# Kernel tuning notes

Measured on AMD Instinct MI355X. Metric: run time of the kernel, lower is better.

## Reference

```python
import jax, jax.numpy as jnp
import numpy as np


def setup_inputs() -> dict:
    key = jax.random.key(0)
    ks = jax.random.split(key, 12)
    S, B, I, H = 1024, 64, 1024, 1024
    stdv = 1.0 / np.sqrt(H)
    def u(k, shape):
        return jax.random.uniform(k, shape, jnp.float32, -stdv, stdv)
    return {
        "input": jax.random.normal(ks[0], (S, B, I), jnp.float32),
        "w_ih_r": u(ks[1], (H, I)),
        "w_hh_r": jax.random.normal(ks[2], (H, H), jnp.float32) * stdv,
        "w_ih_z": u(ks[3], (H, I)),
        "w_hh_z": jax.random.normal(ks[4], (H, H), jnp.float32) * stdv,
        "w_ih_n": u(ks[5], (H, I)),
        "w_hh_n": jax.random.normal(ks[6], (H, H), jnp.float32) * stdv,
        "b_ih_r": u(ks[7], (H,)),
        "b_hh_r": jnp.zeros((H,), jnp.float32),
        "b_ih_z": u(ks[8], (H,)),
        "b_hh_z": jnp.zeros((H,), jnp.float32),
        "b_ih_n": u(ks[9], (H,)),
        "b_hh_n": jnp.zeros((H,), jnp.float32),
    }


def _gru_forward(input, w_ih_r, w_hh_r, w_ih_z, w_hh_z, w_ih_n, w_hh_n,
                 b_ih_r, b_hh_r, b_ih_z, b_hh_z, b_ih_n, b_hh_n):
    S, B, _ = input.shape
    H = w_hh_r.shape[0]
    # Precompute input projections for all timesteps (large batched GEMMs).
    xr = jnp.einsum('sbi,hi->sbh', input, w_ih_r) + b_ih_r  # [S,B,H]
    xz = jnp.einsum('sbi,hi->sbh', input, w_ih_z) + b_ih_z
    xn = jnp.einsum('sbi,hi->sbh', input, w_ih_n) + b_ih_n

    h0 = jnp.zeros((B, H), input.dtype)

    def step(h, xs):
        xr_t, xz_t, xn_t = xs
        r = jax.nn.sigmoid(xr_t + h @ w_hh_r.T + b_hh_r)
        z = jax.nn.sigmoid(xz_t + h @ w_hh_z.T + b_hh_z)
        n = jnp.tanh(xn_t + (r * h) @ w_hh_n.T + b_hh_n)
        h_new = (1.0 - z) * n + z * h
        return h_new, h_new

    h_n, output = jax.lax.scan(step, h0, (xr, xz, xn))
    return output, h_n  # [S,B,H], [B,H]


def reference(input, w_ih_r, w_hh_r, w_ih_z, w_hh_z, w_ih_n, w_hh_n,
              b_ih_r, b_hh_r, b_ih_z, b_hh_z, b_ih_n, b_hh_n):
    return _gru_forward(input, w_ih_r, w_hh_r, w_ih_z, w_hh_z, w_ih_n, w_hh_n,
                        b_ih_r, b_hh_r, b_ih_z, b_hh_z, b_ih_n, b_hh_n)
```

## Files before the change

kernel.cpp:

```cpp
#include <hip/hip_runtime.h>
#include <hip/hip_bf16.h>

typedef __bf16 bf16_t;
typedef __bf16 bf16x8 __attribute__((ext_vector_type(8)));
typedef float  f32x4  __attribute__((ext_vector_type(4)));
typedef unsigned long long u64;

#define S_LEN 1024
#define NBLK  64
#define FLAG_STRIDE 64

__device__ inline f32x4 mfma16(bf16x8 a, bf16x8 b, f32x4 c) {
  return __builtin_amdgcn_mfma_f32_16x16x32_bf16(a, b, c, 0, 0, 0);
}
__device__ inline float fsigmoid(float x) {
  x = fmaxf(-30.f, fminf(30.f, x));
  return 1.f / (1.f + __expf(-x));
}
__device__ inline float ftanh(float x) {
  x = fmaxf(-15.f, fminf(15.f, x));
  float e = __expf(2.f * x);
  return (e - 1.f) / (e + 1.f);
}

__device__ inline void st_coh_bf16(bf16_t* p, float v) {
  bf16_t b = (bf16_t)v;
  __hip_atomic_store((unsigned short*)p, __builtin_bit_cast(unsigned short, b),
                     __ATOMIC_RELAXED, __HIP_MEMORY_SCOPE_AGENT);
}

__device__ __forceinline__ bf16x8 ld_coh(const bf16_t* p) {
  f32x4 r;
  asm volatile("global_load_dwordx4 %0, %1, off sc0 sc1" : "=v"(r) : "v"(p));
  return __builtin_bit_cast(bf16x8, r);
}

__global__ void k_cast_x(const float* __restrict__ x, bf16_t* __restrict__ xb, int n8) {
  int i = blockIdx.x * blockDim.x + threadIdx.x;
  if (i >= n8) return;
  const float4* p = (const float4*)(x + (size_t)i * 8);
  float4 a = p[0], b = p[1];
  bf16x8 o;
  o[0]=(bf16_t)a.x; o[1]=(bf16_t)a.y; o[2]=(bf16_t)a.z; o[3]=(bf16_t)a.w;
  o[4]=(bf16_t)b.x; o[5]=(bf16_t)b.y; o[6]=(bf16_t)b.z; o[7]=(bf16_t)b.w;
  *(bf16x8*)(xb + (size_t)i * 8) = o;
}

__global__ void k_prep_w(const float* __restrict__ wihr, const float* __restrict__ whhr,
                         const float* __restrict__ wihz, const float* __restrict__ whhz,
                         const float* __restrict__ wihn, const float* __restrict__ whhn,
                         const float* __restrict__ bihr, const float* __restrict__ bhhr,
                         const float* __restrict__ bihz, const float* __restrict__ bhhz,
                         const float* __restrict__ bihn, const float* __restrict__ bhhn,
                         bf16_t* __restrict__ wih, bf16_t* __restrict__ whh,
                         float* __restrict__ bias) {
  int i = blockIdx.x * blockDim.x + threadIdx.x;
  const int M = 1024 * 1024;
  if (i < M) {
    wih[i]       = (bf16_t)wihr[i];
    wih[M + i]   = (bf16_t)wihz[i];
    wih[2*M + i] = (bf16_t)wihn[i];
    whh[i]       = (bf16_t)whhr[i];
    whh[M + i]   = (bf16_t)whhz[i];
    whh[2*M + i] = (bf16_t)whhn[i];
  }
  if (i < 1024) {
    bias[i]        = bihr[i] + bhhr[i];
    bias[1024 + i] = bihz[i] + bhhz[i];
    bias[2048 + i] = bihn[i] + bhhn[i];
  }
}

__global__ __launch_bounds__(256) void k_gemm(
    const bf16_t* __restrict__ A, const bf16_t* __restrict__ B,
    const float* __restrict__ bias,
    bf16_t* __restrict__ xrz, float* __restrict__ xn)
{
  __shared__ __align__(16) bf16_t As[128 * 32];
  __shared__ __align__(16) bf16_t Bs[128 * 32];
  const int tid  = threadIdx.x;
  const int lane = tid & 63;
  const int wid  = tid >> 6;
  const int wm   = wid & 1, wn = wid >> 1;
  const int quad = lane >> 4, l15 = lane & 15;
  const int m0 = blockIdx.x * 128;
  const int f0 = blockIdx.y * 128;

  const int r0 = tid >> 2,         o0 = (tid & 3) * 8;
  const int r1 = (tid + 256) >> 2, o1 = ((tid + 256) & 3) * 8;

  const bf16_t* Ag = A + (size_t)m0 * 1024;
  const bf16_t* Bg = B + (size_t)f0 * 1024;

  f32x4 acc[4][4] = {};

  bf16x8 pa0 = *(const bf16x8*)(Ag + r0 * 1024 + o0);
  bf16x8 pa1 = *(const bf16x8*)(Ag + r1 * 1024 + o1);
  bf16x8 pb0 = *(const bf16x8*)(Bg + r0 * 1024 + o0);
  bf16x8 pb1 = *(const bf16x8*)(Bg + r1 * 1024 + o1);

  for (int k0 = 0; k0 < 1024; k0 += 32) {
    __syncthreads();
    *(bf16x8*)&As[r0 * 32 + o0] = pa0;
    *(bf16x8*)&As[r1 * 32 + o1] = pa1;
    *(bf16x8*)&Bs[r0 * 32 + o0] = pb0;
    *(bf16x8*)&Bs[r1 * 32 + o1] = pb1;
    __syncthreads();
    if (k0 + 32 < 1024) {
      const bf16_t* Ag2 = Ag + k0 + 32;
      const bf16_t* Bg2 = Bg + k0 + 32;
      pa0 = *(const bf16x8*)(Ag2 + r0 * 1024 + o0);
      pa1 = *(const bf16x8*)(Ag2 + r1 * 1024 + o1);
      pb0 = *(const bf16x8*)(Bg2 + r0 * 1024 + o0);
      pb1 = *(const bf16x8*)(Bg2 + r1 * 1024 + o1);
    }
    bf16x8 af[4], bfr[4];
#pragma unroll
    for (int t = 0; t < 4; t++) {
      af[t]  = *(const bf16x8*)&As[(wm * 64 + t * 16 + l15) * 32 + quad * 8];
      bfr[t] = *(const bf16x8*)&Bs[(wn * 64 + t * 16 + l15) * 32 + quad * 8];
    }
#pragma unroll
    for (int mt = 0; mt < 4; mt++)
#pragma unroll
      for (int nt = 0; nt < 4; nt++)
        acc[mt][nt] = mfma16(af[mt], bfr[nt], acc[mt][nt]);
  }

  float bcol[4];
#pragma unroll
  for (int nt = 0; nt < 4; nt++) bcol[nt] = bias[f0 + wn * 64 + nt * 16 + l15];

  const bool is_n = (blockIdx.y >= 16);
#pragma unroll
  for (int mt = 0; mt < 4; mt++) {
#pragma unroll
    for (int nt = 0; nt < 4; nt++) {
#pragma unroll
      for (int j = 0; j < 4; j++) {
        int m = m0 + wm * 64 + mt * 16 + quad * 4 + j;
        int f = f0 + wn * 64 + nt * 16 + l15;
        float v = acc[mt][nt][j] + bcol[nt];
        if (!is_n) xrz[(size_t)m * 2048 + f] = (bf16_t)v;
        else       xn[(size_t)m * 1024 + (f - 2048)] = v;
      }
    }
  }
}

__global__ void k_zero_flags(unsigned* f) {
  for (int i = threadIdx.x; i < NBLK * FLAG_STRIDE; i += 256) f[i] = 0;
}

__device__ inline void gridbar(unsigned* flags, int bid, unsigned p) {
  asm volatile("s_waitcnt vmcnt(0)" ::: "memory");
  __syncthreads();
  if (threadIdx.x == 0)
    __hip_atomic_store(&flags[bid * FLAG_STRIDE], p, __ATOMIC_RELAXED,
                       __HIP_MEMORY_SCOPE_AGENT);
  if (threadIdx.x < NBLK) {
    while (__hip_atomic_load(&flags[threadIdx.x * FLAG_STRIDE], __ATOMIC_RELAXED,
                             __HIP_MEMORY_SCOPE_AGENT) < p)
      __builtin_amdgcn_s_sleep(1);
  }
  __syncthreads();
}

__global__ __launch_bounds__(256, 1) void k_gru(
    const bf16_t* __restrict__ xrz,
    const bf16_t* __restrict__ whh,
    float* __restrict__ out,
    bf16_t* __restrict__ hb,
    bf16_t* __restrict__ rh, unsigned* __restrict__ flags)
{
  __shared__ __align__(16) bf16_t wl[48 * 1032];
  const int tid  = threadIdx.x;
  const int bid  = blockIdx.x;
  const int lane = tid & 63;
  const int wid  = tid >> 6;
  const int quad = lane >> 4, l15 = lane & 15;

  for (int i = tid; i < 48 * 128; i += 256) {
    int row = i >> 7;
    int c   = (i & 127) * 8;
    int gr  = (row >> 4) * 1024 + bid * 16 + (row & 15);
    *(bf16x8*)&wl[row * 1032 + c] = *(const bf16x8*)&whh[(size_t)gr * 1024 + c];
  }
  for (int i = tid; i < 64 * 4; i += 256) {
    int b = i >> 2, c = i & 3;
    __hip_atomic_store((u64*)(hb + (size_t)b * 1024 + bid * 16) + c, 0ull,
                       __ATOMIC_RELAXED, __HIP_MEMORY_SCOPE_AGENT);
  }
  gridbar(flags, bid, 1);

  const int abase = (wid * 16 + l15) * 1024 + quad * 8;
  const int fg = bid * 16 + l15;
  unsigned p = 2;

  float hreg[4] = {0.f, 0.f, 0.f, 0.f};
  float xr_pf[4], xz_pf[4], xn_pf[4];
#pragma unroll
  for (int j = 0; j < 4; j++) {
    int b = wid * 16 + quad * 4 + j;
    xr_pf[j] = (float)xrz[(size_t)b * 2048 + fg];
    xz_pf[j] = (float)xrz[(size_t)b * 2048 + 1024 + fg];
    xn_pf[j] = out[(size_t)b * 1024 + fg];
  }

  for (int t = 0; t < S_LEN; t++) {
    const int mrow = t * 64;

    bf16x8 hbuf[32];
    {
      const bf16_t* hrow = hb + abase;
#pragma unroll
      for (int kk = 0; kk < 32; kk++) hbuf[kk] = ld_coh(hrow + kk * 32);
    }
    f32x4 ar = {}, az = {};
    asm volatile("s_waitcnt vmcnt(16)" ::: "memory");
    __builtin_amdgcn_sched_barrier(0);
#pragma unroll
    for (int kk = 0; kk < 16; kk++) {
      bf16x8 br = *(const bf16x8*)&wl[l15 * 1032 + kk * 32 + quad * 8];
      bf16x8 bz = *(const bf16x8*)&wl[(16 + l15) * 1032 + kk * 32 + quad * 8];
      ar = mfma16(hbuf[kk], br, ar);
      az = mfma16(hbuf[kk], bz, az);
    }
    asm volatile("s_waitcnt vmcnt(0)" ::: "memory");
    __builtin_amdgcn_sched_barrier(0);
#pragma unroll
    for (int kk = 16; kk < 32; kk++) {
      bf16x8 br = *(const bf16x8*)&wl[l15 * 1032 + kk * 32 + quad * 8];
      bf16x8 bz = *(const bf16x8*)&wl[(16 + l15) * 1032 + kk * 32 + quad * 8];
      ar = mfma16(hbuf[kk], br, ar);
      az = mfma16(hbuf[kk], bz, az);
    }
    float zreg[4];
#pragma unroll
    for (int j = 0; j < 4; j++) {
      int b = wid * 16 + quad * 4 + j;
      float rv = fsigmoid(xr_pf[j] + ar[j]);
      float zv = fsigmoid(xz_pf[j] + az[j]);
      zreg[j] = zv;
      st_coh_bf16(&rh[b * 1024 + fg], rv * hreg[j]);
    }
    gridbar(flags, bid, p); p++;

    bf16x8 rbuf[32];
    {
      const bf16_t* rrow = rh + abase;
#pragma unroll
      for (int kk = 0; kk < 32; kk++) rbuf[kk] = ld_coh(rrow + kk * 32);
    }
    f32x4 an = {};
    asm volatile("s_waitcnt vmcnt(16)" ::: "memory");
    __builtin_amdgcn_sched_barrier(0);
#pragma unroll
    for (int kk = 0; kk < 16; kk++) {
      bf16x8 bn = *(const bf16x8*)&wl[(32 + l15) * 1032 + kk * 32 + quad * 8];
      an = mfma16(rbuf[kk], bn, an);
    }
    asm volatile("s_waitcnt vmcnt(0)" ::: "memory");
    __builtin_amdgcn_sched_barrier(0);
    float xn_cur[4];
#pragma unroll
    for (int j = 0; j < 4; j++) xn_cur[j] = xn_pf[j];
    if (t + 1 < S_LEN) {
#pragma unroll
      for (int j = 0; j < 4; j++) {
        int b = wid * 16 + quad * 4 + j;
        xr_pf[j] = (float)xrz[(size_t)(mrow + 64 + b) * 2048 + fg];
        xz_pf[j] = (float)xrz[(size_t)(mrow + 64 + b) * 2048 + 1024 + fg];
        xn_pf[j] = out[(size_t)(mrow + 64 + b) * 1024 + fg];
      }
    }
#pragma unroll
    for (int kk = 16; kk < 32; kk++) {
      bf16x8 bn = *(const bf16x8*)&wl[(32 + l15) * 1032 + kk * 32 + quad * 8];
      an = mfma16(rbuf[kk], bn, an);
    }
#pragma unroll
    for (int j = 0; j < 4; j++) {
      int b = wid * 16 + quad * 4 + j;
      size_t oix = (size_t)(mrow + b) * 1024 + fg;
      float nv  = ftanh(xn_cur[j] + an[j]);
      float hv  = (1.f - zreg[j]) * nv + zreg[j] * hreg[j];
      hreg[j] = hv;
      out[oix] = hv;
      st_coh_bf16(&hb[b * 1024 + fg], hv);
      if (t == S_LEN - 1) out[(size_t)S_LEN * 64 * 1024 + b * 1024 + fg] = hv;
    }
    if (t + 1 < S_LEN) { gridbar(flags, bid, p); p++; }
  }
}

extern "C" void kernel_launch(void* const* d_in, const int* in_sizes, int n_in,
                              void* d_out, int out_size, void* d_ws, size_t ws_size,
                              hipStream_t stream) {
  const float* x    = (const float*)d_in[0];
  const float* wihr = (const float*)d_in[1];
  const float* whhr = (const float*)d_in[2];
  const float* wihz = (const float*)d_in[3];
  const float* whhz = (const float*)d_in[4];
  const float* wihn = (const float*)d_in[5];
  const float* whhn = (const float*)d_in[6];
  const float* bihr = (const float*)d_in[7];
  const float* bhhr = (const float*)d_in[8];
  const float* bihz = (const float*)d_in[9];
  const float* bhhz = (const float*)d_in[10];
  const float* bihn = (const float*)d_in[11];
  const float* bhhn = (const float*)d_in[12];
  float* out = (float*)d_out;

  char* w = (char*)d_ws;
  bf16_t*  Xb    = (bf16_t*)(w);
  bf16_t*  xrz   = (bf16_t*)(w + 134217728);
  bf16_t*  wih   = (bf16_t*)(w + 402653184);
  bf16_t*  whh   = (bf16_t*)(w + 408944640);
  float*   bias  = (float*) (w + 415236096);
  unsigned* flags = (unsigned*)(w + 415248384);
  bf16_t*  hb    = (bf16_t*)(w + 415510528);
  bf16_t*  rh    = (bf16_t*)(w + 415641600);

  k_cast_x<<<dim3(8388608 / 256), dim3(256), 0, stream>>>(x, Xb, 8388608);
  k_prep_w<<<dim3(1048576 / 256), dim3(256), 0, stream>>>(
      wihr, whhr, wihz, whhz, wihn, whhn,
      bihr, bhhr, bihz, bhhz, bihn, bhhn, wih, whh, bias);
  k_gemm<<<dim3(512, 24), dim3(256), 0, stream>>>(Xb, wih, bias, xrz, out);
  k_zero_flags<<<dim3(1), dim3(256), 0, stream>>>(flags);
  k_gru<<<dim3(NBLK), dim3(256), 0, stream>>>(xrz, whh, out, hb, rh, flags);
}
```

Measured before the change: 13.60 ms.

## Replace block-wide grid barrier with per-wave flag barriers and split arrive/wait

Replaces the block-level grid barrier (syncthreads plus one flag per block) with per-wavefront flags. Each wave publishes its own flag and polls only the matching flags of the other blocks' same-index wave, using a wave-wide all-reduce and no __syncthreads. This works because each wave only consumes the batch rows its counterpart waves produce. The second barrier per step is split into arrive and wait, so the next timestep's xr/xz/xn prefetch loads are issued between them. The intent is to remove intra-block sync overhead and hide prefetch latency behind barrier waiting, at the cost of four times as many flags and more subtle correctness reasoning.

```diff
diff --git a/kernel.cpp b/kernel.cpp
--- a/kernel.cpp
+++ b/kernel.cpp
@@ -8,7 +8,7 @@
 
 #define S_LEN 1024
 #define NBLK  64
-#define FLAG_STRIDE 64
+#define FLAG_STRIDE 32
 
 __device__ inline f32x4 mfma16(bf16x8 a, bf16x8 b, f32x4 c) {
   return __builtin_amdgcn_mfma_f32_16x16x32_bf16(a, b, c, 0, 0, 0);
@@ -149,21 +149,7 @@
 }
 
 __global__ void k_zero_flags(unsigned* f) {
-  for (int i = threadIdx.x; i < NBLK * FLAG_STRIDE; i += 256) f[i] = 0;
-}
-
-__device__ inline void gridbar(unsigned* flags, int bid, unsigned p) {
-  asm volatile("s_waitcnt vmcnt(0)" ::: "memory");
-  __syncthreads();
-  if (threadIdx.x == 0)
-    __hip_atomic_store(&flags[bid * FLAG_STRIDE], p, __ATOMIC_RELAXED,
-                       __HIP_MEMORY_SCOPE_AGENT);
-  if (threadIdx.x < NBLK) {
-    while (__hip_atomic_load(&flags[threadIdx.x * FLAG_STRIDE], __ATOMIC_RELAXED,
-                             __HIP_MEMORY_SCOPE_AGENT) < p)
-      __builtin_amdgcn_s_sleep(1);
-  }
-  __syncthreads();
+  for (int i = threadIdx.x; i < 4 * NBLK * FLAG_STRIDE; i += 256) f[i] = 0;
 }
 
 __global__ __launch_bounds__(256, 1) void k_gru(
@@ -186,12 +172,22 @@
     int gr  = (row >> 4) * 1024 + bid * 16 + (row & 15);
     *(bf16x8*)&wl[row * 1032 + c] = *(const bf16x8*)&whh[(size_t)gr * 1024 + c];
   }
-  for (int i = tid; i < 64 * 4; i += 256) {
-    int b = i >> 2, c = i & 3;
-    __hip_atomic_store((u64*)(hb + (size_t)b * 1024 + bid * 16) + c, 0ull,
-                       __ATOMIC_RELAXED, __HIP_MEMORY_SCOPE_AGENT);
-  }
-  gridbar(flags, bid, 1);
+#pragma unroll
+  for (int j = 0; j < 4; j++) {
+    int b = wid * 16 + quad * 4 + j;
+    st_coh_bf16(&hb[b * 1024 + bid * 16 + l15], 0.f);
+  }
+  __syncthreads();
+
+  unsigned* myflag = flags + (wid * NBLK + bid) * FLAG_STRIDE;
+  const unsigned* mypoll = flags + (wid * NBLK + lane) * FLAG_STRIDE;
+
+  asm volatile("s_waitcnt vmcnt(0)" ::: "memory");
+  if (lane == 0)
+    __hip_atomic_store(myflag, 1u, __ATOMIC_RELAXED, __HIP_MEMORY_SCOPE_AGENT);
+  while (!__all(__hip_atomic_load(mypoll, __ATOMIC_RELAXED,
+                                  __HIP_MEMORY_SCOPE_AGENT) >= 1u))
+    __builtin_amdgcn_s_sleep(1);
 
   const int abase = (wid * 16 + l15) * 1024 + quad * 8;
   const int fg = bid * 16 + l15;
@@ -244,7 +240,13 @@
       zreg[j] = zv;
       st_coh_bf16(&rh[b * 1024 + fg], rv * hreg[j]);
     }
-    gridbar(flags, bid, p); p++;
+    asm volatile("s_waitcnt vmcnt(0)" ::: "memory");
+    if (lane == 0)
+      __hip_atomic_store(myflag, p, __ATOMIC_RELAXED, __HIP_MEMORY_SCOPE_AGENT);
+    while (!__all(__hip_atomic_load(mypoll, __ATOMIC_RELAXED,
+                                    __HIP_MEMORY_SCOPE_AGENT) >= p))
+      __builtin_amdgcn_s_sleep(1);
+    p++;
 
     bf16x8 rbuf[32];
     {
@@ -262,10 +264,26 @@
     }
     asm volatile("s_waitcnt vmcnt(0)" ::: "memory");
     __builtin_amdgcn_sched_barrier(0);
-    float xn_cur[4];
-#pragma unroll
-    for (int j = 0; j < 4; j++) xn_cur[j] = xn_pf[j];
+#pragma unroll
+    for (int kk = 16; kk < 32; kk++) {
+      bf16x8 bn = *(const bf16x8*)&wl[(32 + l15) * 1032 + kk * 32 + quad * 8];
+      an = mfma16(rbuf[kk], bn, an);
+    }
+#pragma unroll
+    for (int j = 0; j < 4; j++) {
+      int b = wid * 16 + quad * 4 + j;
+      size_t oix = (size_t)(mrow + b) * 1024 + fg;
+      float nv  = ftanh(xn_pf[j] + an[j]);
+      float hv  = (1.f - zreg[j]) * nv + zreg[j] * hreg[j];
+      hreg[j] = hv;
+      out[oix] = hv;
+      st_coh_bf16(&hb[b * 1024 + fg], hv);
+      if (t == S_LEN - 1) out[(size_t)S_LEN * 64 * 1024 + b * 1024 + fg] = hv;
+    }
     if (t + 1 < S_LEN) {
+      asm volatile("s_waitcnt vmcnt(0)" ::: "memory");
+      if (lane == 0)
+        __hip_atomic_store(myflag, p, __ATOMIC_RELAXED, __HIP_MEMORY_SCOPE_AGENT);
 #pragma unroll
       for (int j = 0; j < 4; j++) {
         int b = wid * 16 + quad * 4 + j;
@@ -273,24 +291,11 @@
         xz_pf[j] = (float)xrz[(size_t)(mrow + 64 + b) * 2048 + 1024 + fg];
         xn_pf[j] = out[(size_t)(mrow + 64 + b) * 1024 + fg];
       }
-    }
-#pragma unroll
-    for (int kk = 16; kk < 32; kk++) {
-      bf16x8 bn = *(const bf16x8*)&wl[(32 + l15) * 1032 + kk * 32 + quad * 8];
-      an = mfma16(rbuf[kk], bn, an);
-    }
-#pragma unroll
-    for (int j = 0; j < 4; j++) {
-      int b = wid * 16 + quad * 4 + j;
-      size_t oix = (size_t)(mrow + b) * 1024 + fg;
-      float nv  = ftanh(xn_cur[j] + an[j]);
-      float hv  = (1.f - zreg[j]) * nv + zreg[j] * hreg[j];
-      hreg[j] = hv;
-      out[oix] = hv;
-      st_coh_bf16(&hb[b * 1024 + fg], hv);
-      if (t == S_LEN - 1) out[(size_t)S_LEN * 64 * 1024 + b * 1024 + fg] = hv;
-    }
-    if (t + 1 < S_LEN) { gridbar(flags, bid, p); p++; }
+      while (!__all(__hip_atomic_load(mypoll, __ATOMIC_RELAXED,
+                                      __HIP_MEMORY_SCOPE_AGENT) >= p))
+        __builtin_amdgcn_s_sleep(1);
+      p++;
+    }
   }
 }
 
```

Result: no change. 13.37 ms (-1.7%).
